# Kernel tuning notes

Measured on AMD Instinct MI355X. Metric: run time of the kernel, lower is better.

## Reference

```python
import jax, jax.numpy as jnp
import numpy as np

IN_FEATS = 128
HIDDEN = 32
OUT_CLASSES = 2
N_NODES = 100000
N_EDGES = 625000


def setup_inputs() -> dict:
    key = jax.random.key(0)
    k1, k2, k3, k4, k5, k6, k7 = jax.random.split(key, 7)
    src_nodes = jax.random.randint(k1, (N_EDGES,), 0, N_NODES, dtype=jnp.int64 if jax.config.jax_enable_x64 else jnp.int32)
    dst_nodes = jax.random.randint(k2, (N_EDGES,), 0, N_NODES, dtype=jnp.int64 if jax.config.jax_enable_x64 else jnp.int32)
    node_embed = jax.random.normal(k3, (N_NODES, IN_FEATS), dtype=jnp.float32)
    # Linear params (torch nn.Linear default init: U(-1/sqrt(fan_in), 1/sqrt(fan_in)))
    lim1 = 1.0 / np.sqrt(2 * IN_FEATS)
    W1 = jax.random.uniform(k4, (HIDDEN, 2 * IN_FEATS), jnp.float32, -lim1, lim1)
    b1 = jax.random.uniform(k5, (HIDDEN,), jnp.float32, -lim1, lim1)
    lim2 = 1.0 / np.sqrt(HIDDEN)
    W2 = jax.random.uniform(k6, (OUT_CLASSES, HIDDEN), jnp.float32, -lim2, lim2)
    b2 = jax.random.uniform(k7, (OUT_CLASSES,), jnp.float32, -lim2, lim2)
    return {"src_nodes": src_nodes, "dst_nodes": dst_nodes, "node_embed": node_embed,
            "W1": W1, "b1": b1, "W2": W2, "b2": b2}


def reference(src_nodes, dst_nodes, node_embed, W1, b1, W2, b2):
    # Gather endpoint embeddings: [E, F] each
    src_e = node_embed[src_nodes]
    dst_e = node_embed[dst_nodes]
    # Avoid materializing the concat explicitly in the GEMM by splitting W1:
    # fc1(cat([s, d])) == s @ W1[:, :F].T + d @ W1[:, F:].T + b1
    W1s, W1d = W1[:, :IN_FEATS], W1[:, IN_FEATS:]
    h = jax.nn.relu(src_e @ W1s.T + dst_e @ W1d.T + b1)  # [E, 32]
    logits = h @ W2.T + b2  # [E, out_classes]
    return logits
```

## Files before the change

kernel.cpp:

```cpp
#include <hip/hip_runtime.h>

#define IN_FEATS 128
#define HIDDEN 32

typedef short v8s __attribute__((ext_vector_type(8)));
typedef unsigned short u16x8 __attribute__((ext_vector_type(8)));
typedef float v4f __attribute__((ext_vector_type(4)));

__device__ __forceinline__ unsigned short f2bf(float x) {
    union { float f; unsigned int u; } v; v.f = x;
    const unsigned int r = v.u + 0x7fffu + ((v.u >> 16) & 1u);
    return (unsigned short)(r >> 16);
}
__device__ __forceinline__ float bf2f(unsigned short b) {
    union { float f; unsigned int u; } v; v.u = ((unsigned int)b) << 16;
    return v.f;
}

__global__ __launch_bounds__(256, 4) void precompute_P_mfma(
    const float* __restrict__ embed,
    const float* __restrict__ W1,
    unsigned short* __restrict__ P,
    int n_nodes)
{
    __shared__ unsigned short sBhi[8192];
    __shared__ unsigned short sBlo[8192];

    const int t    = threadIdx.x;
    const int lane = t & 63;
    const int wave = t >> 6;

#pragma unroll
    for (int g0 = 0; g0 < 1024; g0 += 256) {
        const int g   = g0 + t;
        const int gl  = g & 63;
        const int ks  = (g >> 6) & 3;
        const int nb  = g >> 8;
        const int u   = nb * 16 + (gl & 15);
        const int k0  = ks * 32 + ((gl >> 4) & 3) * 8;
        const float* wp = W1 + (u & 31) * (2 * IN_FEATS) + (u >> 5) * IN_FEATS + k0;
        const float4 x0 = *reinterpret_cast<const float4*>(wp);
        const float4 x1 = *reinterpret_cast<const float4*>(wp + 4);
        const float xs[8] = {x0.x, x0.y, x0.z, x0.w, x1.x, x1.y, x1.z, x1.w};
        v8s h, l;
#pragma unroll
        for (int j = 0; j < 8; ++j) {
            const unsigned short hb = f2bf(xs[j]);
            h[j] = (short)hb;
            l[j] = (short)f2bf(xs[j] - bf2f(hb));
        }
        *reinterpret_cast<v8s*>(sBhi + g * 8) = h;
        *reinterpret_cast<v8s*>(sBlo + g * 8) = l;
    }
    __syncthreads();

    const int last = n_nodes - 1;
    const int grp  = lane >> 4;

#pragma unroll
    for (int sub = 0; sub < 2; ++sub) {
        const int node0 = blockIdx.x * 128 + wave * 32 + sub * 16;
        if (node0 >= n_nodes) break;
        const int row = min(node0 + (lane & 15), last);

        v8s ahi[4], alo[4];
#pragma unroll
        for (int ks = 0; ks < 4; ++ks) {
            const float* ap = embed + (size_t)row * IN_FEATS + ks * 32 + grp * 8;
            const float4 x0 = *reinterpret_cast<const float4*>(ap);
            const float4 x1 = *reinterpret_cast<const float4*>(ap + 4);
            const float xs[8] = {x0.x, x0.y, x0.z, x0.w, x1.x, x1.y, x1.z, x1.w};
            v8s h, l;
#pragma unroll
            for (int j = 0; j < 8; ++j) {
                const unsigned short hb = f2bf(xs[j]);
                h[j] = (short)hb;
                l[j] = (short)f2bf(xs[j] - bf2f(hb));
            }
            ahi[ks] = h;
            alo[ks] = l;
        }

#pragma unroll
        for (int nb = 0; nb < 4; ++nb) {
            v8s bhi[4], blo[4];
#pragma unroll
            for (int ks = 0; ks < 4; ++ks) {
                const int fi = ((nb * 4 + ks) * 64 + lane) * 8;
                bhi[ks] = *reinterpret_cast<const v8s*>(sBhi + fi);
                blo[ks] = *reinterpret_cast<const v8s*>(sBlo + fi);
            }
            v4f acc = {0.f, 0.f, 0.f, 0.f};
#pragma unroll
            for (int ks = 0; ks < 4; ++ks) {
                acc = __builtin_amdgcn_mfma_f32_16x16x32_bf16(ahi[ks], bhi[ks], acc, 0, 0, 0);
                acc = __builtin_amdgcn_mfma_f32_16x16x32_bf16(ahi[ks], blo[ks], acc, 0, 0, 0);
                acc = __builtin_amdgcn_mfma_f32_16x16x32_bf16(alo[ks], bhi[ks], acc, 0, 0, 0);
            }
            const int u = nb * 16 + (lane & 15);
#pragma unroll
            for (int r = 0; r < 4; ++r) {
                const int n = node0 + grp * 4 + r;
                if (n < n_nodes)
                    P[(size_t)n * 64 + u] = f2bf(acc[r]);
            }
        }
    }
}

__global__ __launch_bounds__(256) void edge_classify_bf16(
    const int* __restrict__ src,
    const int* __restrict__ dst,
    const unsigned short* __restrict__ P,
    const float* __restrict__ b1,
    const float* __restrict__ W2,
    const float* __restrict__ b2,
    float* __restrict__ out,
    int n_edges)
{
    const int t  = threadIdx.x;
    const int q  = t & 3;
    const int e0 = blockIdx.x * 128 + (t >> 2);
    const int e1 = e0 + 64;
    if (e0 >= n_edges) return;
    const bool has1 = (e1 < n_edges);

    const int s0 = src[e0], d0 = dst[e0];
    const int s1 = has1 ? src[e1] : s0;
    const int d1 = has1 ? dst[e1] : d0;

    const u16x8 ps0 = *reinterpret_cast<const u16x8*>(P + (size_t)s0 * 64 + q * 8);
    const u16x8 pd0 = *reinterpret_cast<const u16x8*>(P + (size_t)d0 * 64 + 32 + q * 8);
    const u16x8 ps1 = *reinterpret_cast<const u16x8*>(P + (size_t)s1 * 64 + q * 8);
    const u16x8 pd1 = *reinterpret_cast<const u16x8*>(P + (size_t)d1 * 64 + 32 + q * 8);

    const float4 b1a = *reinterpret_cast<const float4*>(b1 + q * 8);
    const float4 b1b = *reinterpret_cast<const float4*>(b1 + q * 8 + 4);
    const float4 w0a = *reinterpret_cast<const float4*>(W2 + q * 8);
    const float4 w0b = *reinterpret_cast<const float4*>(W2 + q * 8 + 4);
    const float4 w1a = *reinterpret_cast<const float4*>(W2 + HIDDEN + q * 8);
    const float4 w1b = *reinterpret_cast<const float4*>(W2 + HIDDEN + q * 8 + 4);
    const float bb1[8] = {b1a.x, b1a.y, b1a.z, b1a.w, b1b.x, b1b.y, b1b.z, b1b.w};
    const float ww0[8] = {w0a.x, w0a.y, w0a.z, w0a.w, w0b.x, w0b.y, w0b.z, w0b.w};
    const float ww1[8] = {w1a.x, w1a.y, w1a.z, w1a.w, w1b.x, w1b.y, w1b.z, w1b.w};

    float a0 = 0.f, a1 = 0.f, c0 = 0.f, c1 = 0.f;
#pragma unroll
    for (int j = 0; j < 8; ++j) {
        float h0 = bf2f(ps0[j]) + bf2f(pd0[j]) + bb1[j];
        float h1 = bf2f(ps1[j]) + bf2f(pd1[j]) + bb1[j];
        h0 = fmaxf(h0, 0.f);
        h1 = fmaxf(h1, 0.f);
        a0 = fmaf(h0, ww0[j], a0);
        a1 = fmaf(h0, ww1[j], a1);
        c0 = fmaf(h1, ww0[j], c0);
        c1 = fmaf(h1, ww1[j], c1);
    }
    a0 += __shfl_xor(a0, 1); a0 += __shfl_xor(a0, 2);
    a1 += __shfl_xor(a1, 1); a1 += __shfl_xor(a1, 2);
    c0 += __shfl_xor(c0, 1); c0 += __shfl_xor(c0, 2);
    c1 += __shfl_xor(c1, 1); c1 += __shfl_xor(c1, 2);
    if (q == 0) {
        *reinterpret_cast<float2*>(out + (size_t)e0 * 2) =
            make_float2(a0 + b2[0], a1 + b2[1]);
        if (has1)
            *reinterpret_cast<float2*>(out + (size_t)e1 * 2) =
                make_float2(c0 + b2[0], c1 + b2[1]);
    }
}

__global__ __launch_bounds__(256) void edge_direct(
    const int* __restrict__ src, const int* __restrict__ dst,
    const float* __restrict__ embed,
    const float* __restrict__ W1, const float* __restrict__ b1,
    const float* __restrict__ W2, const float* __restrict__ b2,
    float* __restrict__ out, int n_edges)
{
    const int e = blockIdx.x * 256 + threadIdx.x;
    if (e >= n_edges) return;
    const int s = src[e], d = dst[e];
    const float* se = embed + (size_t)s * IN_FEATS;
    const float* de = embed + (size_t)d * IN_FEATS;

    float acc[HIDDEN];
#pragma unroll
    for (int hh = 0; hh < HIDDEN; ++hh) acc[hh] = b1[hh];

    for (int c = 0; c < 4; ++c) {
        float es[32], ed[32];
#pragma unroll
        for (int q = 0; q < 8; ++q) {
            const float4 v = *reinterpret_cast<const float4*>(se + c * 32 + q * 4);
            es[q*4+0] = v.x; es[q*4+1] = v.y; es[q*4+2] = v.z; es[q*4+3] = v.w;
            const float4 u = *reinterpret_cast<const float4*>(de + c * 32 + q * 4);
            ed[q*4+0] = u.x; ed[q*4+1] = u.y; ed[q*4+2] = u.z; ed[q*4+3] = u.w;
        }
#pragma unroll
        for (int hh = 0; hh < HIDDEN; ++hh) {
            float acch = acc[hh];
#pragma unroll
            for (int k = 0; k < 32; ++k) {
                acch = fmaf(es[k], W1[hh * 256 + c * 32 + k], acch);
                acch = fmaf(ed[k], W1[hh * 256 + 128 + c * 32 + k], acch);
            }
            acc[hh] = acch;
        }
    }

    float l0 = b2[0], l1 = b2[1];
#pragma unroll
    for (int hh = 0; hh < HIDDEN; ++hh) {
        const float hv = fmaxf(acc[hh], 0.f);
        l0 = fmaf(hv, W2[hh], l0);
        l1 = fmaf(hv, W2[HIDDEN + hh], l1);
    }
    *reinterpret_cast<float2*>(out + (size_t)e * 2) = make_float2(l0, l1);
}

extern "C" void kernel_launch(void* const* d_in, const int* in_sizes, int n_in,
                              void* d_out, int out_size, void* d_ws, size_t ws_size,
                              hipStream_t stream)
{
    const int*   src = (const int*)d_in[0];
    const int*   dst = (const int*)d_in[1];
    const float* emb = (const float*)d_in[2];
    const float* W1  = (const float*)d_in[3];
    const float* b1  = (const float*)d_in[4];
    const float* W2  = (const float*)d_in[5];
    const float* b2  = (const float*)d_in[6];
    float* out = (float*)d_out;

    const int n_edges = in_sizes[0];
    const int n_nodes = in_sizes[2] / IN_FEATS;

    const size_t p_bytes = (size_t)n_nodes * 64 * sizeof(unsigned short);

    if (ws_size >= p_bytes) {
        unsigned short* P = (unsigned short*)d_ws;
        const int nb_nodes = (n_nodes + 127) / 128;
        precompute_P_mfma<<<nb_nodes, 256, 0, stream>>>(emb, W1, P, n_nodes);
        const int nb_edges = (n_edges + 127) / 128;
        edge_classify_bf16<<<nb_edges, 256, 0, stream>>>(src, dst, P, b1, W2, b2, out, n_edges);
    } else {
        const int nb_edges = (n_edges + 255) / 256;
        edge_direct<<<nb_edges, 256, 0, stream>>>(src, dst, emb, W1, b1, W2, b2, out, n_edges);
    }
}
```

Baseline: 41.09 us.

## Fold b1 into precomputed P, use hardware bf16 convert, 4 edges per quad

Replaces the software round-to-nearest bf16 conversion with the HIP __float2bfloat16 intrinsic, which may map to a hardware convert. Adds b1 into the source half of the precomputed P table so the edge kernel no longer loads or adds it. The edge kernel now processes four edges per thread quad instead of two, halving the block count and issuing more independent gathers per thread to raise memory-level parallelism. The trade-off is higher register use per thread, and a second bf16 rounding of the biased value stored in P.

```diff
diff --git a/kernel.cpp b/kernel.cpp
--- a/kernel.cpp
+++ b/kernel.cpp
@@ -1,4 +1,5 @@
 #include <hip/hip_runtime.h>
+#include <hip/hip_bf16.h>
 
 #define IN_FEATS 128
 #define HIDDEN 32
@@ -7,12 +8,11 @@
 typedef unsigned short u16x8 __attribute__((ext_vector_type(8)));
 typedef float v4f __attribute__((ext_vector_type(4)));
 
-__device__ __forceinline__ unsigned short f2bf(float x) {
-    union { float f; unsigned int u; } v; v.f = x;
-    const unsigned int r = v.u + 0x7fffu + ((v.u >> 16) & 1u);
-    return (unsigned short)(r >> 16);
-}
-__device__ __forceinline__ float bf2f(unsigned short b) {
+__device__ __forceinline__ short hw_f2bf(float x) {
+    __hip_bfloat16 b = __float2bfloat16(x);
+    return *reinterpret_cast<short*>(&b);
+}
+__device__ __forceinline__ float bf2f_raw(unsigned short b) {
     union { float f; unsigned int u; } v; v.u = ((unsigned int)b) << 16;
     return v.f;
 }
@@ -20,6 +20,7 @@
 __global__ __launch_bounds__(256, 4) void precompute_P_mfma(
     const float* __restrict__ embed,
     const float* __restrict__ W1,
+    const float* __restrict__ b1,
     unsigned short* __restrict__ P,
     int n_nodes)
 {
@@ -45,14 +46,17 @@
         v8s h, l;
 #pragma unroll
         for (int j = 0; j < 8; ++j) {
-            const unsigned short hb = f2bf(xs[j]);
-            h[j] = (short)hb;
-            l[j] = (short)f2bf(xs[j] - bf2f(hb));
+            const short hb = hw_f2bf(xs[j]);
+            h[j] = hb;
+            l[j] = hw_f2bf(xs[j] - bf2f_raw((unsigned short)hb));
         }
         *reinterpret_cast<v8s*>(sBhi + g * 8) = h;
         *reinterpret_cast<v8s*>(sBlo + g * 8) = l;
     }
     __syncthreads();
+
+    const float bias_nb0 = b1[lane & 15];
+    const float bias_nb1 = b1[16 + (lane & 15)];
 
     const int last = n_nodes - 1;
     const int grp  = lane >> 4;
@@ -73,9 +77,9 @@
             v8s h, l;
 #pragma unroll
             for (int j = 0; j < 8; ++j) {
-                const unsigned short hb = f2bf(xs[j]);
-                h[j] = (short)hb;
-                l[j] = (short)f2bf(xs[j] - bf2f(hb));
+                const short hb = hw_f2bf(xs[j]);
+                h[j] = hb;
+                l[j] = hw_f2bf(xs[j] - bf2f_raw((unsigned short)hb));
             }
             ahi[ks] = h;
             alo[ks] = l;
@@ -97,12 +101,13 @@
                 acc = __builtin_amdgcn_mfma_f32_16x16x32_bf16(ahi[ks], blo[ks], acc, 0, 0, 0);
                 acc = __builtin_amdgcn_mfma_f32_16x16x32_bf16(alo[ks], bhi[ks], acc, 0, 0, 0);
             }
+            const float bias = (nb == 0) ? bias_nb0 : (nb == 1) ? bias_nb1 : 0.f;
             const int u = nb * 16 + (lane & 15);
 #pragma unroll
             for (int r = 0; r < 4; ++r) {
                 const int n = node0 + grp * 4 + r;
                 if (n < n_nodes)
-                    P[(size_t)n * 64 + u] = f2bf(acc[r]);
+                    P[(size_t)n * 64 + u] = (unsigned short)hw_f2bf(acc[r] + bias);
             }
         }
     }
@@ -112,60 +117,66 @@
     const int* __restrict__ src,
     const int* __restrict__ dst,
     const unsigned short* __restrict__ P,
-    const float* __restrict__ b1,
     const float* __restrict__ W2,
     const float* __restrict__ b2,
     float* __restrict__ out,
     int n_edges)
 {
-    const int t  = threadIdx.x;
-    const int q  = t & 3;
-    const int e0 = blockIdx.x * 128 + (t >> 2);
-    const int e1 = e0 + 64;
+    const int t   = threadIdx.x;
+    const int q   = t & 3;
+    const int qid = t >> 2;
+    const int e0  = blockIdx.x * 256 + qid;
     if (e0 >= n_edges) return;
-    const bool has1 = (e1 < n_edges);
-
-    const int s0 = src[e0], d0 = dst[e0];
-    const int s1 = has1 ? src[e1] : s0;
-    const int d1 = has1 ? dst[e1] : d0;
-
-    const u16x8 ps0 = *reinterpret_cast<const u16x8*>(P + (size_t)s0 * 64 + q * 8);
-    const u16x8 pd0 = *reinterpret_cast<const u16x8*>(P + (size_t)d0 * 64 + 32 + q * 8);
-    const u16x8 ps1 = *reinterpret_cast<const u16x8*>(P + (size_t)s1 * 64 + q * 8);
-    const u16x8 pd1 = *reinterpret_cast<const u16x8*>(P + (size_t)d1 * 64 + 32 + q * 8);
-
-    const float4 b1a = *reinterpret_cast<const float4*>(b1 + q * 8);
-    const float4 b1b = *reinterpret_cast<const float4*>(b1 + q * 8 + 4);
+
+    int se[4], de[4];
+#pragma unroll
+    for (int k = 0; k < 4; ++k) {
+        const int e  = e0 + k * 64;
+        const int ec = (e < n_edges) ? e : e0;
+        se[k] = src[ec];
+        de[k] = dst[ec];
+    }
+
+    u16x8 ps[4], pd[4];
+#pragma unroll
+    for (int k = 0; k < 4; ++k) {
+        ps[k] = *reinterpret_cast<const u16x8*>(P + (size_t)se[k] * 64 + q * 8);
+        pd[k] = *reinterpret_cast<const u16x8*>(P + (size_t)de[k] * 64 + 32 + q * 8);
+    }
+
     const float4 w0a = *reinterpret_cast<const float4*>(W2 + q * 8);
     const float4 w0b = *reinterpret_cast<const float4*>(W2 + q * 8 + 4);
     const float4 w1a = *reinterpret_cast<const float4*>(W2 + HIDDEN + q * 8);
     const float4 w1b = *reinterpret_cast<const float4*>(W2 + HIDDEN + q * 8 + 4);
-    const float bb1[8] = {b1a.x, b1a.y, b1a.z, b1a.w, b1b.x, b1b.y, b1b.z, b1b.w};
     const float ww0[8] = {w0a.x, w0a.y, w0a.z, w0a.w, w0b.x, w0b.y, w0b.z, w0b.w};
     const float ww1[8] = {w1a.x, w1a.y, w1a.z, w1a.w, w1b.x, w1b.y, w1b.z, w1b.w};
 
-    float a0 = 0.f, a1 = 0.f, c0 = 0.f, c1 = 0.f;
-#pragma unroll
-    for (int j = 0; j < 8; ++j) {
-        float h0 = bf2f(ps0[j]) + bf2f(pd0[j]) + bb1[j];
-        float h1 = bf2f(ps1[j]) + bf2f(pd1[j]) + bb1[j];
-        h0 = fmaxf(h0, 0.f);
-        h1 = fmaxf(h1, 0.f);
-        a0 = fmaf(h0, ww0[j], a0);
-        a1 = fmaf(h0, ww1[j], a1);
-        c0 = fmaf(h1, ww0[j], c0);
-        c1 = fmaf(h1, ww1[j], c1);
-    }
-    a0 += __shfl_xor(a0, 1); a0 += __shfl_xor(a0, 2);
-    a1 += __shfl_xor(a1, 1); a1 += __shfl_xor(a1, 2);
-    c0 += __shfl_xor(c0, 1); c0 += __shfl_xor(c0, 2);
-    c1 += __shfl_xor(c1, 1); c1 += __shfl_xor(c1, 2);
+    float l0[4] = {0.f, 0.f, 0.f, 0.f};
+    float l1[4] = {0.f, 0.f, 0.f, 0.f};
+#pragma unroll
+    for (int k = 0; k < 4; ++k) {
+#pragma unroll
+        for (int j = 0; j < 8; ++j) {
+            float h = bf2f_raw(ps[k][j]) + bf2f_raw(pd[k][j]);
+            h = fmaxf(h, 0.f);
+            l0[k] = fmaf(h, ww0[j], l0[k]);
+            l1[k] = fmaf(h, ww1[j], l1[k]);
+        }
+    }
+#pragma unroll
+    for (int k = 0; k < 4; ++k) {
+        l0[k] += __shfl_xor(l0[k], 1); l0[k] += __shfl_xor(l0[k], 2);
+        l1[k] += __shfl_xor(l1[k], 1); l1[k] += __shfl_xor(l1[k], 2);
+    }
     if (q == 0) {
-        *reinterpret_cast<float2*>(out + (size_t)e0 * 2) =
-            make_float2(a0 + b2[0], a1 + b2[1]);
-        if (has1)
-            *reinterpret_cast<float2*>(out + (size_t)e1 * 2) =
-                make_float2(c0 + b2[0], c1 + b2[1]);
+        const float bias0 = b2[0], bias1 = b2[1];
+#pragma unroll
+        for (int k = 0; k < 4; ++k) {
+            const int e = e0 + k * 64;
+            if (e < n_edges)
+                *reinterpret_cast<float2*>(out + (size_t)e * 2) =
+                    make_float2(l0[k] + bias0, l1[k] + bias1);
+        }
     }
 }
 
@@ -238,9 +249,9 @@
     if (ws_size >= p_bytes) {
         unsigned short* P = (unsigned short*)d_ws;
         const int nb_nodes = (n_nodes + 127) / 128;
-        precompute_P_mfma<<<nb_nodes, 256, 0, stream>>>(emb, W1, P, n_nodes);
-        const int nb_edges = (n_edges + 127) / 128;
-        edge_classify_bf16<<<nb_edges, 256, 0, stream>>>(src, dst, P, b1, W2, b2, out, n_edges);
+        precompute_P_mfma<<<nb_nodes, 256, 0, stream>>>(emb, W1, b1, P, n_nodes);
+        const int nb_edges = (n_edges + 255) / 256;
+        edge_classify_bf16<<<nb_edges, 256, 0, stream>>>(src, dst, P, W2, b2, out, n_edges);
     } else {
         const int nb_edges = (n_edges + 255) / 256;
         edge_direct<<<nb_edges, 256, 0, stream>>>(src, dst, emb, W1, b1, W2, b2, out, n_edges);
```

New measurement: 41.41 us. About the same (+0.8%).
